# Performance work log

Hardware: AMD Instinct MI355X
Metric: run time of the kernel (lower is better)

## Reference

```python
import jax, jax.numpy as jnp
import numpy as np

N = 50000   # num_entities
R = 16      # num_relations
B = 8       # num_bases
D = 128     # embedding_dim == hidden_dim
E = 625000  # num_edges
EPS = 1e-5  # LayerNorm eps


def _rgcn_layer(x, row, col, edge_type, bases, coef, selfw, bias):
    # weights[r] = sum_b coef[r,b] * bases[b]  (rio). We apply bases to x first
    # (cheaper: N*B*d*d) then mix by coefficients, since (x @ W[r])[col] == x[col] @ W[r].
    z = jnp.einsum('ni,bio->bno', x, bases)          # [B,N,D]
    y = jnp.einsum('rb,bno->rno', coef, z)           # [R,N,D] == x @ W[r]
    msg = y[edge_type, col]                          # [E,D] per-edge messages
    key = edge_type * N + row                        # combined (relation,node) segment id
    agg = jax.ops.segment_sum(msg, key, num_segments=R * N).reshape(R, N, D)
    deg = jax.ops.segment_sum(jnp.ones((msg.shape[0],), x.dtype), key,
                              num_segments=R * N).reshape(R, N, 1)
    agg = (agg / jnp.maximum(deg, 1.0)).sum(0)       # per-relation mean-agg, summed over r
    return x @ selfw + agg + bias


def _layernorm(x, g, b):
    m = x.mean(-1, keepdims=True)
    v = ((x - m) ** 2).mean(-1, keepdims=True)
    return (x - m) * jax.lax.rsqrt(v + EPS) * g + b


def setup_inputs() -> dict:
    key = jax.random.key(0)
    ks = jax.random.split(key, 10)
    s = 1.0 / np.sqrt(D)
    sb = 1.0 / np.sqrt(B)
    return {
        'edge_index': jax.random.randint(ks[0], (2, E), 0, N),
        'edge_type': jax.random.randint(ks[1], (E,), 0, R),
        'emb': jax.random.normal(ks[2], (N, D), jnp.float32) * s,
        'bases1': jax.random.normal(ks[3], (B, D, D), jnp.float32) * s,
        'coef1': jax.random.normal(ks[4], (R, B), jnp.float32) * sb,
        'selfw1': jax.random.normal(ks[5], (D, D), jnp.float32) * s,
        'bias1': jnp.zeros((D,), jnp.float32),
        'g1': jnp.ones((D,), jnp.float32),
        'b1': jnp.zeros((D,), jnp.float32),
        'bases2': jax.random.normal(ks[6], (B, D, D), jnp.float32) * s,
        'coef2': jax.random.normal(ks[7], (R, B), jnp.float32) * sb,
        'selfw2': jax.random.normal(ks[8], (D, D), jnp.float32) * s,
        'bias2': jnp.zeros((D,), jnp.float32),
        'g2': jnp.ones((D,), jnp.float32),
        'b2': jnp.zeros((D,), jnp.float32),
    }


def reference(edge_index, edge_type, emb, bases1, coef1, selfw1, bias1, g1, b1,
              bases2, coef2, selfw2, bias2, g2, b2):
    row, col = edge_index[0], edge_index[1]
    x = emb
    # layer 1 (dropout is identity in eval)
    x = _rgcn_layer(x, row, col, edge_type, bases1, coef1, selfw1, bias1)
    x = jax.nn.relu(_layernorm(x, g1, b1))
    # layer 2
    x = _rgcn_layer(x, row, col, edge_type, bases2, coef2, selfw2, bias2)
    x = jax.nn.relu(_layernorm(x, g2, b2))
    return x
```

## Files before the change

kernel.cpp:

```cpp
#include <hip/hip_runtime.h>
#include <hip/hip_bf16.h>


static constexpr int kDim = 128;
static constexpr int kRel = 16;
static constexpr int kBas = 8;
static constexpr int kSeg = kBas + 1;

typedef __attribute__((ext_vector_type(8))) short bf16x8;
typedef __attribute__((ext_vector_type(4))) float f32x4;

static __device__ __forceinline__ float bf2f_rg(unsigned short h) {
    return __uint_as_float(((unsigned)h) << 16);
}
static __device__ __forceinline__ unsigned short f2bf_rg(float f) {
    unsigned u = __float_as_uint(f);
    u = u + 0x7fffu + ((u >> 16) & 1u);
    return (unsigned short)(u >> 16);
}

static __device__ __forceinline__ void gload_lds16(const void* g, void* l) {
    __builtin_amdgcn_global_load_lds(
        (const __attribute__((address_space(1))) unsigned*)g,
        (__attribute__((address_space(3))) unsigned*)l, 16, 0, 0);
}

static __device__ __forceinline__ int flag_from(const unsigned short* x, int lane) {
    unsigned e0 = ((unsigned)x[lane] >> 7) & 0xFFu;
    unsigned e1 = ((unsigned)x[lane + 64] >> 7) & 0xFFu;
    int bad = (e0 >= 0x86u) || (e1 >= 0x86u);
    return (__ballot(bad) != 0ull) ? 1 : 0;
}

__global__ void RGCNEncoder_89962384982025_kernel(unsigned* p, int n) {
    int i = blockIdx.x * 256 + threadIdx.x;
    if (i < n) p[i] = 0x3F803F80u;
}

__global__ void prep_rg(const void* xraw, unsigned short* xout, int nelem,
                        int* cnt, int n16) {
    __shared__ int fsh;
    if (threadIdx.x < 64) {
        int fl = flag_from((const unsigned short*)xraw, threadIdx.x);
        if (threadIdx.x == 0) fsh = fl;
    }
    __syncthreads();
    int f = fsh;
    int i = blockIdx.x * 256 + threadIdx.x;
    if (i < n16) cnt[i] = 0;
    if (i < nelem) {
        if (f)
            xout[i] = f2bf_rg(((const float*)xraw)[i]);
        else
            xout[i] = ((const unsigned short*)xraw)[i];
    }
}

__global__ void count_rg(const int* ei, const int* et, int* cnt, int E) {
    int e = blockIdx.x * 256 + threadIdx.x;
    if (e < E) atomicAdd(&cnt[ei[e] * kRel + et[e]], 1);
}

__global__ void scanA_rg(const int* cnt, int* rowptr, int* bsum, int n) {
    __shared__ int sh[256];
    int tid = threadIdx.x;
    int i = blockIdx.x * 256 + tid;
    int v = (i < n) ? cnt[i] : 0;
    sh[tid] = v;
    __syncthreads();
    for (int off = 1; off < 256; off <<= 1) {
        int t = (tid >= off) ? sh[tid - off] : 0;
        __syncthreads();
        sh[tid] += t;
        __syncthreads();
    }
    if (i < n) rowptr[i + 1] = sh[tid];
    if (tid == 255) bsum[blockIdx.x] = sh[255];
}
__global__ void scanB_rg(int* bsum, int nb) {
    __shared__ int partial[256];
    int tid = threadIdx.x;
    int chunk = (nb + 255) / 256;
    int s0 = tid * chunk;
    int s1 = min(s0 + chunk, nb);
    int sum = 0;
    for (int i = s0; i < s1; ++i) sum += bsum[i];
    partial[tid] = sum;
    __syncthreads();
    for (int off = 1; off < 256; off <<= 1) {
        int t = (tid >= off) ? partial[tid - off] : 0;
        __syncthreads();
        partial[tid] += t;
        __syncthreads();
    }
    int run = (tid == 0) ? 0 : partial[tid - 1];
    for (int i = s0; i < s1; ++i) { int v = bsum[i]; bsum[i] = run; run += v; }
}
__global__ void scanC_rg(int* rowptr, const int* bsum, int n) {
    int i = blockIdx.x * 256 + threadIdx.x;
    if (i < n) rowptr[i + 1] += bsum[blockIdx.x];
    if (i == 0) rowptr[0] = 0;
}

__global__ void fill_rg(const int* ei, const int* et, const int* rowptr,
                        int* cnt, int* pcols, int E) {
    int e = blockIdx.x * 256 + threadIdx.x;
    if (e < E) {
        int rel = et[e];
        int key = ei[e] * kRel + rel;
        int old = atomicSub(&cnt[key], 1);
        pcols[rowptr[key] + old - 1] = ei[E + e] | (rel << 26);
    }
}

__global__ void wall2_rg(const void* bases1, const void* coef1, const void* selfw1,
                         const void* bases2, const void* coef2, const void* selfw2,
                         const unsigned short* emb, unsigned short* wallT,
                         float* coefw) {
    __shared__ int fsh;
    if (threadIdx.x < 64) {
        int fl = flag_from(emb, threadIdx.x);
        if (threadIdx.x == 0) fsh = fl;
    }
    __syncthreads();
    int f = fsh;
    int bi = blockIdx.x;
    int layer = (bi >= kSeg * 64) ? 1 : 0;
    int lb = bi - layer * kSeg * 64;
    const void* bases = layer ? bases2 : bases1;
    const void* coef  = layer ? coef2  : coef1;
    const void* selfw = layer ? selfw2 : selfw1;
    int idx = lb * 256 + threadIdx.x;
    int b = idx >> 14;
    int o = (idx >> 7) & 127;
    int k = idx & 127;
    if (lb == 0 && threadIdx.x < kRel * kBas) {
        coefw[layer * 128 + threadIdx.x] =
            f ? ((const float*)coef)[threadIdx.x]
              : bf2f_rg(((const unsigned short*)coef)[threadIdx.x]);
    }
    unsigned short* wout = wallT + (size_t)layer * kSeg * 16384;
    if (b < kBas) {
        float bv = f ? ((const float*)bases)[b * 16384 + k * 128 + o]
                     : bf2f_rg(((const unsigned short*)bases)[b * 16384 + k * 128 + o]);
        wout[idx] = f2bf_rg(bv);
    } else {
        float sv = f ? ((const float*)selfw)[k * 128 + o]
                     : bf2f_rg(((const unsigned short*)selfw)[k * 128 + o]);
        wout[idx] = f2bf_rg(sv);
    }
}

__global__ __launch_bounds__(256) void agg2_rg(const int* rowptr2, const int* pcols,
                                               const unsigned short* xsrc,
                                               const float* coefw,
                                               unsigned short* Gall, int N) {
    __shared__ float csh[kRel * kBas];
    if (threadIdx.x < kRel * kBas) csh[threadIdx.x] = coefw[threadIdx.x];
    __syncthreads();
    int wv = threadIdx.x >> 6;
    int lane = threadIdx.x & 63;
    int n = blockIdx.x * 4 + wv;
    if (n >= N) return;
    const int s = rowptr2[n * kRel];
    const int e = rowptr2[n * kRel + kRel];
    const unsigned short* xl = xsrc + 2 * lane;
    float g0[kBas], g1[kBas];
#pragma unroll
    for (int b = 0; b < kBas; ++b) { g0[b] = 0.f; g1[b] = 0.f; }
    float s0 = 0.f, s1 = 0.f;
    int cur = -1, cnt = 0;
    auto flush = [&]() {
        float w = __builtin_amdgcn_rcpf((float)cnt);
        float t0 = s0 * w, t1 = s1 * w;
        const float* cr = csh + cur * kBas;
#pragma unroll
        for (int b = 0; b < kBas; ++b) {
            float c = cr[b];
            g0[b] += c * t0;
            g1[b] += c * t1;
        }
        s0 = 0.f; s1 = 0.f; cnt = 0;
    };
    for (int base = s; base < e; base += 64) {
        int m = e - base;
        if (m > 64) m = 64;
        int pk = 0;
        if (base + lane < e) pk = pcols[base + lane];
        int i = 0;
        for (; i + 4 <= m; i += 4) {
            int v0 = __builtin_amdgcn_readlane(pk, i);
            int v1 = __builtin_amdgcn_readlane(pk, i + 1);
            int v2 = __builtin_amdgcn_readlane(pk, i + 2);
            int v3 = __builtin_amdgcn_readlane(pk, i + 3);
            unsigned u0 = *(const unsigned*)(xl + (size_t)(v0 & 0x03FFFFFF) * 128);
            unsigned u1 = *(const unsigned*)(xl + (size_t)(v1 & 0x03FFFFFF) * 128);
            unsigned u2 = *(const unsigned*)(xl + (size_t)(v2 & 0x03FFFFFF) * 128);
            unsigned u3 = *(const unsigned*)(xl + (size_t)(v3 & 0x03FFFFFF) * 128);
            int r0 = (int)((unsigned)v0 >> 26);
            int r1 = (int)((unsigned)v1 >> 26);
            int r2 = (int)((unsigned)v2 >> 26);
            int r3 = (int)((unsigned)v3 >> 26);
            if (r0 != cur) { if (cnt) flush(); cur = r0; }
            s0 += __uint_as_float(u0 << 16); s1 += __uint_as_float(u0 & 0xffff0000u); ++cnt;
            if (r1 != cur) { flush(); cur = r1; }
            s0 += __uint_as_float(u1 << 16); s1 += __uint_as_float(u1 & 0xffff0000u); ++cnt;
            if (r2 != cur) { flush(); cur = r2; }
            s0 += __uint_as_float(u2 << 16); s1 += __uint_as_float(u2 & 0xffff0000u); ++cnt;
            if (r3 != cur) { flush(); cur = r3; }
            s0 += __uint_as_float(u3 << 16); s1 += __uint_as_float(u3 & 0xffff0000u); ++cnt;
        }
        for (; i < m; ++i) {
            int v = __builtin_amdgcn_readlane(pk, i);
            unsigned u = *(const unsigned*)(xl + (size_t)(v & 0x03FFFFFF) * 128);
            int rel = (int)((unsigned)v >> 26);
            if (rel != cur) { if (cnt) flush(); cur = rel; }
            s0 += __uint_as_float(u << 16);
            s1 += __uint_as_float(u & 0xffff0000u);
            ++cnt;
        }
    }
    if (cnt) flush();
    unsigned short* grow = Gall + (size_t)n * 128 + 2 * lane;
    const size_t plane = (size_t)N * 128;
#pragma unroll
    for (int b = 0; b < kBas; ++b) {
        unsigned outp = (unsigned)f2bf_rg(g0[b]) | ((unsigned)f2bf_rg(g1[b]) << 16);
        *(unsigned*)(grow + (size_t)b * plane) = outp;
    }
}

__global__ __launch_bounds__(512, 4) void fusegemm_rg(const unsigned short* Gall,
                                                      const unsigned short* x,
                                                      const unsigned short* wallT,
                                                      const void* bias, const void* gw,
                                                      const void* bw,
                                                      const unsigned short* emb,
                                                      unsigned short* out_b, float* out_f,
                                                      int ofp32, int M) {
    __shared__ __align__(16) unsigned short As[2][128][128];
    __shared__ float pS[128][8];
    __shared__ float pQ[128][8];
    __shared__ float mrs[128][2];
    __shared__ int fsh;
    const int m0 = blockIdx.x * 128;
    const int tid = threadIdx.x;
    const int wave = tid >> 6;
    const int lane = tid & 63;
    const int wn = wave * 16;
    const int lrow = lane & 15;
    const int lq = lane >> 4;
    if (tid < 64) {
        int fl = flag_from(emb, tid);
        if (tid == 0) fsh = fl;
    }

    auto stage = [&](int seg, int buf) {
        const char* srcb = (seg < kBas)
            ? (const char*)(Gall + (size_t)seg * (size_t)M * 128)
            : (const char*)x;
#pragma unroll
        for (int it = 0; it < 4; ++it) {
            int gi = it * 512 + tid;
            int row = gi >> 4;
            int c = ((gi & 15) << 4) ^ ((row & 7) << 4);
            int gr = m0 + row;
            if (gr > M - 1) gr = M - 1;
            const char* src = srcb + (size_t)gr * 256 + (size_t)c;
            unsigned short* ldst = &As[buf][0][0] + gi * 8;
            gload_lds16(src, ldst);
        }
    };

    f32x4 acc[8] = {};
    stage(0, 0);
    __syncthreads();
    int cur = 0;
    for (int seg = 0; seg < kSeg; ++seg) {
        const unsigned short* Bsrc = wallT + (size_t)seg * 16384
                                   + (size_t)(wn + lrow) * 128;
        bf16x8 b[4];
#pragma unroll
        for (int kk4 = 0; kk4 < 4; ++kk4)
            b[kk4] = *(const bf16x8*)(Bsrc + kk4 * 32 + lq * 8);
        __builtin_amdgcn_sched_barrier(0);
        if (seg < kSeg - 1) stage(seg + 1, cur ^ 1);
#pragma unroll
        for (int kk4 = 0; kk4 < 4; ++kk4) {
#pragma unroll
            for (int mt = 0; mt < 8; ++mt) {
                int row = mt * 16 + lrow;
                int cb = (kk4 * 64 + lq * 16) ^ ((row & 7) << 4);
                bf16x8 a = *(const bf16x8*)((const char*)&As[cur][0][0]
                                            + row * 256 + cb);
                acc[mt] = __builtin_amdgcn_mfma_f32_16x16x32_bf16(
                    a, b[kk4], acc[mt], 0, 0, 0);
            }
        }
        asm volatile("s_waitcnt vmcnt(0)" ::: "memory");
        __builtin_amdgcn_s_barrier();
        cur ^= 1;
    }

    const int f = fsh;
    const int gc = wn + lrow;
    float bv, gv, betav;
    if (f) {
        bv = ((const float*)bias)[gc];
        gv = ((const float*)gw)[gc];
        betav = ((const float*)bw)[gc];
    } else {
        bv = bf2f_rg(((const unsigned short*)bias)[gc]);
        gv = bf2f_rg(((const unsigned short*)gw)[gc]);
        betav = bf2f_rg(((const unsigned short*)bw)[gc]);
    }
#pragma unroll
    for (int mt = 0; mt < 8; ++mt)
#pragma unroll
        for (int i = 0; i < 4; ++i) {
            float v = acc[mt][i] + bv;
            acc[mt][i] = v;
            float sv = v, qv = v * v;
            for (int o = 1; o < 16; o <<= 1) {
                sv += __shfl_xor(sv, o);
                qv += __shfl_xor(qv, o);
            }
            if (lrow == 0) {
                int row = mt * 16 + lq * 4 + i;
                pS[row][wave] = sv;
                pQ[row][wave] = qv;
            }
        }
    __syncthreads();
    if (tid < 128) {
        float s8 = 0.f, q8 = 0.f;
#pragma unroll
        for (int w = 0; w < 8; ++w) { s8 += pS[tid][w]; q8 += pQ[tid][w]; }
        float mean = s8 * (1.0f / 128.0f);
        float var = q8 * (1.0f / 128.0f) - mean * mean;
        mrs[tid][0] = mean;
        mrs[tid][1] = rsqrtf(var + 1e-5f);
    }
    __syncthreads();
#pragma unroll
    for (int mt = 0; mt < 8; ++mt)
#pragma unroll
        for (int i = 0; i < 4; ++i) {
            int row = mt * 16 + lq * 4 + i;
            int gr = m0 + row;
            if (gr < M) {
                float o = fmaxf((acc[mt][i] - mrs[row][0]) * mrs[row][1] * gv + betav,
                                0.f);
                if (ofp32)
                    out_f[(size_t)gr * 128 + gc] = o;
                else
                    out_b[(size_t)gr * 128 + gc] = f2bf_rg(o);
            }
        }
}

extern "C" void kernel_launch(void* const* d_in, const int* in_sizes, int n_in,
                              void* d_out, int out_size, void* d_ws, size_t ws_size,
                              hipStream_t stream) {
    const int* ei = (const int*)d_in[0];
    const int* et = (const int*)d_in[1];
    const void* emb    = d_in[2];
    const void* bases1 = d_in[3];
    const void* coef1  = d_in[4];
    const void* selfw1 = d_in[5];
    const void* bias1  = d_in[6];
    const void* g1     = d_in[7];
    const void* b1     = d_in[8];
    const void* bases2 = d_in[9];
    const void* coef2  = d_in[10];
    const void* selfw2 = d_in[11];
    const void* bias2  = d_in[12];
    const void* g2     = d_in[13];
    const void* b2     = d_in[14];

    const int E = in_sizes[1];
    const int N = out_size / kDim;
    const int n16 = N * kRel;
    const int nsb = (n16 + 255) / 256;

    char* ws = (char*)d_ws;
    size_t off = 0;
    float* coefw = (float*)(ws + off); off += 1024;
    int* rowptr2 = (int*)(ws + off); off += (((size_t)n16 + 1) * 4 + 255) & ~(size_t)255;
    int* cnt     = (int*)(ws + off); off += ((size_t)n16 * 4 + 255) & ~(size_t)255;
    int* bsum    = (int*)(ws + off); off += ((size_t)nsb * 4 + 255) & ~(size_t)255;
    int* pcols   = (int*)(ws + off); off += ((size_t)E * 4 + 255) & ~(size_t)255;
    unsigned short* wallT = (unsigned short*)(ws + off);
    off += ((size_t)2 * kSeg * 16384 * 2 + 255) & ~(size_t)255;
    unsigned short* xin  = (unsigned short*)(ws + off);
    off += ((size_t)N * 128 * 2 + 255) & ~(size_t)255;
    unsigned short* xmid = (unsigned short*)(ws + off);
    off += ((size_t)N * 128 * 2 + 255) & ~(size_t)255;
    unsigned short* Gall = (unsigned short*)(ws + off);
    (void)n_in; (void)ws_size;

    const int eblk = (E + 255) / 256;
    const int mblk128 = (N + 127) / 128;
    const int ablk = (N + 3) / 4;
    const int nelem = N * 128;
    const unsigned short* embh = (const unsigned short*)emb;

    RGCNEncoder_89962384982025_kernel<<<1, 256, 0, stream>>>((unsigned*)d_out, 256);

    prep_rg<<<(nelem + 255) / 256, 256, 0, stream>>>(emb, xin, nelem, cnt, n16);

    count_rg<<<eblk, 256, 0, stream>>>(ei, et, cnt, E);
    scanA_rg<<<nsb, 256, 0, stream>>>(cnt, rowptr2, bsum, n16);
    scanB_rg<<<1, 256, 0, stream>>>(bsum, nsb);
    scanC_rg<<<nsb, 256, 0, stream>>>(rowptr2, bsum, n16);
    fill_rg<<<eblk, 256, 0, stream>>>(ei, et, rowptr2, cnt, pcols, E);

    wall2_rg<<<2 * kSeg * 64, 256, 0, stream>>>(bases1, coef1, selfw1,
                                                bases2, coef2, selfw2,
                                                embh, wallT, coefw);

    agg2_rg<<<ablk, 256, 0, stream>>>(rowptr2, pcols, xin, coefw, Gall, N);
    fusegemm_rg<<<mblk128, 512, 0, stream>>>(Gall, xin, wallT, bias1, g1, b1, embh,
                                             xmid, (float*)nullptr, 0, N);

    agg2_rg<<<ablk, 256, 0, stream>>>(rowptr2, pcols, xmid, coefw + 128, Gall, N);
    fusegemm_rg<<<mblk128, 512, 0, stream>>>(Gall, xmid, wallT + (size_t)kSeg * 16384,
                                             bias2, g2, b2, embh,
                                             (unsigned short*)nullptr, (float*)d_out,
                                             1, N);
}
```

Baseline: 359.2 us.

## Restructure fused GEMM+LayerNorm so each wave owns 32 full rows

Result: slower. 424.5 us (+18.2%).

```diff
diff --git a/kernel.cpp b/kernel.cpp
--- a/kernel.cpp
+++ b/kernel.cpp
@@ -230,131 +230,110 @@
     }
 }
 
-__global__ __launch_bounds__(512, 4) void fusegemm_rg(const unsigned short* Gall,
-                                                      const unsigned short* x,
-                                                      const unsigned short* wallT,
-                                                      const void* bias, const void* gw,
-                                                      const void* bw,
-                                                      const unsigned short* emb,
-                                                      unsigned short* out_b, float* out_f,
-                                                      int ofp32, int M) {
-    __shared__ __align__(16) unsigned short As[2][128][128];
-    __shared__ float pS[128][8];
-    __shared__ float pQ[128][8];
-    __shared__ float mrs[128][2];
-    __shared__ int fsh;
-    const int m0 = blockIdx.x * 128;
+__global__ __launch_bounds__(128) void fusegemm_rg(const unsigned short* Gall,
+                                                   const unsigned short* x,
+                                                   const unsigned short* wallT,
+                                                   const void* bias, const void* gw,
+                                                   const void* bw,
+                                                   const unsigned short* emb,
+                                                   unsigned short* out_b, float* out_f,
+                                                   int ofp32, int M) {
+    __shared__ __align__(16) unsigned short As[2][32][128];
     const int tid = threadIdx.x;
-    const int wave = tid >> 6;
+    const int wv = tid >> 6;
     const int lane = tid & 63;
-    const int wn = wave * 16;
     const int lrow = lane & 15;
     const int lq = lane >> 4;
-    if (tid < 64) {
-        int fl = flag_from(emb, tid);
-        if (tid == 0) fsh = fl;
-    }
-
-    auto stage = [&](int seg, int buf) {
+    const int r0 = (blockIdx.x * 2 + wv) * 32;
+    unsigned short* myA = &As[wv][0][0];
+    const int f = flag_from(emb, lane);
+
+    f32x4 acc[2][8] = {};
+    for (int seg = 0; seg < kSeg; ++seg) {
         const char* srcb = (seg < kBas)
             ? (const char*)(Gall + (size_t)seg * (size_t)M * 128)
             : (const char*)x;
 #pragma unroll
-        for (int it = 0; it < 4; ++it) {
-            int gi = it * 512 + tid;
+        for (int it = 0; it < 8; ++it) {
+            int gi = it * 64 + lane;
             int row = gi >> 4;
             int c = ((gi & 15) << 4) ^ ((row & 7) << 4);
-            int gr = m0 + row;
+            int gr = r0 + row;
             if (gr > M - 1) gr = M - 1;
-            const char* src = srcb + (size_t)gr * 256 + (size_t)c;
-            unsigned short* ldst = &As[buf][0][0] + gi * 8;
-            gload_lds16(src, ldst);
-        }
-    };
-
-    f32x4 acc[8] = {};
-    stage(0, 0);
-    __syncthreads();
-    int cur = 0;
-    for (int seg = 0; seg < kSeg; ++seg) {
-        const unsigned short* Bsrc = wallT + (size_t)seg * 16384
-                                   + (size_t)(wn + lrow) * 128;
-        bf16x8 b[4];
+            gload_lds16(srcb + (size_t)gr * 256 + (size_t)c, myA + gi * 8);
+        }
+        asm volatile("s_waitcnt vmcnt(0)" ::: "memory");
+        bf16x8 a[4][2];
 #pragma unroll
         for (int kk4 = 0; kk4 < 4; ++kk4)
-            b[kk4] = *(const bf16x8*)(Bsrc + kk4 * 32 + lq * 8);
-        __builtin_amdgcn_sched_barrier(0);
-        if (seg < kSeg - 1) stage(seg + 1, cur ^ 1);
-#pragma unroll
-        for (int kk4 = 0; kk4 < 4; ++kk4) {
-#pragma unroll
-            for (int mt = 0; mt < 8; ++mt) {
+#pragma unroll
+            for (int mt = 0; mt < 2; ++mt) {
                 int row = mt * 16 + lrow;
                 int cb = (kk4 * 64 + lq * 16) ^ ((row & 7) << 4);
-                bf16x8 a = *(const bf16x8*)((const char*)&As[cur][0][0]
-                                            + row * 256 + cb);
-                acc[mt] = __builtin_amdgcn_mfma_f32_16x16x32_bf16(
-                    a, b[kk4], acc[mt], 0, 0, 0);
+                a[kk4][mt] = *(const bf16x8*)((const char*)myA + row * 256 + cb);
             }
-        }
-        asm volatile("s_waitcnt vmcnt(0)" ::: "memory");
-        __builtin_amdgcn_s_barrier();
-        cur ^= 1;
-    }
-
-    const int f = fsh;
-    const int gc = wn + lrow;
-    float bv, gv, betav;
-    if (f) {
-        bv = ((const float*)bias)[gc];
-        gv = ((const float*)gw)[gc];
-        betav = ((const float*)bw)[gc];
-    } else {
-        bv = bf2f_rg(((const unsigned short*)bias)[gc]);
-        gv = bf2f_rg(((const unsigned short*)gw)[gc]);
-        betav = bf2f_rg(((const unsigned short*)bw)[gc]);
-    }
-#pragma unroll
-    for (int mt = 0; mt < 8; ++mt)
+        const unsigned short* Bseg = wallT + (size_t)seg * 16384;
+#pragma unroll
+        for (int nt = 0; nt < 8; ++nt) {
+            const unsigned short* Bsrc = Bseg + (size_t)(nt * 16 + lrow) * 128 + lq * 8;
+            bf16x8 bb[4];
+#pragma unroll
+            for (int kk4 = 0; kk4 < 4; ++kk4)
+                bb[kk4] = *(const bf16x8*)(Bsrc + kk4 * 32);
+#pragma unroll
+            for (int kk4 = 0; kk4 < 4; ++kk4)
+#pragma unroll
+                for (int mt = 0; mt < 2; ++mt)
+                    acc[mt][nt] = __builtin_amdgcn_mfma_f32_16x16x32_bf16(
+                        a[kk4][mt], bb[kk4], acc[mt][nt], 0, 0, 0);
+        }
+    }
+
+    float bv[8], gv[8], betav[8];
+#pragma unroll
+    for (int nt = 0; nt < 8; ++nt) {
+        int gc = nt * 16 + lrow;
+        if (f) {
+            bv[nt] = ((const float*)bias)[gc];
+            gv[nt] = ((const float*)gw)[gc];
+            betav[nt] = ((const float*)bw)[gc];
+        } else {
+            bv[nt] = bf2f_rg(((const unsigned short*)bias)[gc]);
+            gv[nt] = bf2f_rg(((const unsigned short*)gw)[gc]);
+            betav[nt] = bf2f_rg(((const unsigned short*)bw)[gc]);
+        }
+    }
+#pragma unroll
+    for (int mt = 0; mt < 2; ++mt)
 #pragma unroll
         for (int i = 0; i < 4; ++i) {
-            float v = acc[mt][i] + bv;
-            acc[mt][i] = v;
-            float sv = v, qv = v * v;
+            float sv = 0.f, qv = 0.f;
+#pragma unroll
+            for (int nt = 0; nt < 8; ++nt) {
+                float v = acc[mt][nt][i] + bv[nt];
+                acc[mt][nt][i] = v;
+                sv += v;
+                qv += v * v;
+            }
             for (int o = 1; o < 16; o <<= 1) {
                 sv += __shfl_xor(sv, o);
                 qv += __shfl_xor(qv, o);
             }
-            if (lrow == 0) {
-                int row = mt * 16 + lq * 4 + i;
-                pS[row][wave] = sv;
-                pQ[row][wave] = qv;
-            }
-        }
-    __syncthreads();
-    if (tid < 128) {
-        float s8 = 0.f, q8 = 0.f;
-#pragma unroll
-        for (int w = 0; w < 8; ++w) { s8 += pS[tid][w]; q8 += pQ[tid][w]; }
-        float mean = s8 * (1.0f / 128.0f);
-        float var = q8 * (1.0f / 128.0f) - mean * mean;
-        mrs[tid][0] = mean;
-        mrs[tid][1] = rsqrtf(var + 1e-5f);
-    }
-    __syncthreads();
-#pragma unroll
-    for (int mt = 0; mt < 8; ++mt)
-#pragma unroll
-        for (int i = 0; i < 4; ++i) {
-            int row = mt * 16 + lq * 4 + i;
-            int gr = m0 + row;
+            float mean = sv * (1.0f / 128.0f);
+            float var = qv * (1.0f / 128.0f) - mean * mean;
+            float rs = rsqrtf(var + 1e-5f);
+            int gr = r0 + mt * 16 + lq * 4 + i;
             if (gr < M) {
-                float o = fmaxf((acc[mt][i] - mrs[row][0]) * mrs[row][1] * gv + betav,
-                                0.f);
-                if (ofp32)
-                    out_f[(size_t)gr * 128 + gc] = o;
-                else
-                    out_b[(size_t)gr * 128 + gc] = f2bf_rg(o);
+#pragma unroll
+                for (int nt = 0; nt < 8; ++nt) {
+                    int gc = nt * 16 + lrow;
+                    float o = fmaxf((acc[mt][nt][i] - mean) * rs * gv[nt] + betav[nt],
+                                    0.f);
+                    if (ofp32)
+                        out_f[(size_t)gr * 128 + gc] = o;
+                    else
+                        out_b[(size_t)gr * 128 + gc] = f2bf_rg(o);
+                }
             }
         }
 }
@@ -400,7 +379,7 @@
     (void)n_in; (void)ws_size;
 
     const int eblk = (E + 255) / 256;
-    const int mblk128 = (N + 127) / 128;
+    const int gblk = (N + 63) / 64;
     const int ablk = (N + 3) / 4;
     const int nelem = N * 128;
     const unsigned short* embh = (const unsigned short*)emb;
@@ -420,12 +399,12 @@
                                                 embh, wallT, coefw);
 
     agg2_rg<<<ablk, 256, 0, stream>>>(rowptr2, pcols, xin, coefw, Gall, N);
-    fusegemm_rg<<<mblk128, 512, 0, stream>>>(Gall, xin, wallT, bias1, g1, b1, embh,
-                                             xmid, (float*)nullptr, 0, N);
+    fusegemm_rg<<<gblk, 128, 0, stream>>>(Gall, xin, wallT, bias1, g1, b1, embh,
+                                          xmid, (float*)nullptr, 0, N);
 
     agg2_rg<<<ablk, 256, 0, stream>>>(rowptr2, pcols, xmid, coefw + 128, Gall, N);
-    fusegemm_rg<<<mblk128, 512, 0, stream>>>(Gall, xmid, wallT + (size_t)kSeg * 16384,
-                                             bias2, g2, b2, embh,
-                                             (unsigned short*)nullptr, (float*)d_out,
-                                             1, N);
-}
+    fusegemm_rg<<<gblk, 128, 0, stream>>>(Gall, xmid, wallT + (size_t)kSeg * 16384,
+                                          bias2, g2, b2, embh,
+                                          (unsigned short*)nullptr, (float*)d_out,
+                                          1, N);
+}
```
